# Kernel tuning notes

Measured on AMD Instinct MI355X. Metric: run time of the kernel, lower is better.

The kernel has to match this reference:

```python
import jax, jax.numpy as jnp
import numpy as np

DT = 0.01  # time_delta from init
SIGMA, RHO, BETA = 10.0, 28.0, 8.0 / 3.0  # Lorenz parameters for self.function


def setup_inputs() -> dict:
    key = jax.random.key(0)
    # traj: [T, len_var, B] ensemble of trajectory states over time
    traj = jax.random.normal(key, (2048, 3, 8192), dtype=jnp.float32)
    return {"traj": traj}


def _jacobian(state):
    # state: [V, B] -> discrete tangent map I + DT * J_lorenz(state), shape [B, V, V]
    x, y, z = state[0], state[1], state[2]
    zero = jnp.zeros_like(x)
    one = jnp.ones_like(x)
    J = jnp.stack([
        jnp.stack([-SIGMA * one, SIGMA * one, zero], axis=-1),
        jnp.stack([RHO - z, -one, -x], axis=-1),
        jnp.stack([y, x, -BETA * one], axis=-1),
    ], axis=-2)  # [B, V, V]
    return jnp.eye(3, dtype=state.dtype) + DT * J


def _gram_schmidt_rows(M):
    # Row-wise Gram-Schmidt + normalization, exactly as the torch gram_schmidt
    # (in-place slicing makes it modified GS against already-orthogonalized rows)
    # followed by normalization(). M: [B, V, V]. Returns (Q [B,V,V], lognorms [V,B]).
    V = M.shape[-2]
    rows, lognorms = [], []
    for k in range(V):
        r = M[..., k, :]
        for q in rows:  # q already unit-norm -> projection coeff is just q.r
            r = r - jnp.sum(q * r, axis=-1, keepdims=True) * q
        n = jnp.sqrt(jnp.sum(r * r, axis=-1, keepdims=True))
        rows.append(r / n)
        lognorms.append(jnp.log(n[..., 0]))
    return jnp.stack(rows, axis=-2), jnp.stack(lognorms, axis=0)


def reference(traj):
    T, V, B = traj.shape
    Q0 = jnp.broadcast_to(jnp.eye(V, dtype=traj.dtype), (B, V, V))

    def step(Q, state):
        M = jnp.einsum('bij,bjk->bik', _jacobian(state), Q)  # eye = Jaco @ eye
        Qn, ln = _gram_schmidt_rows(M)
        return Qn, ln

    _, lns = jax.lax.scan(step, Q0, traj)  # lns: [T, V, B]
    # Running-average recurrence L_{k+1} = (L_k*k*dt + log n_k)/((k+1)*dt)
    # telescopes exactly to sum_k log(n_k) / (T * dt).
    return jnp.sum(lns, axis=0) / (T * DT)  # [V, B] Lyapunov spectrum per trajectory
```

## Files before the change

kernel.cpp:

```cpp
#include <hip/hip_runtime.h>

#define T_STEPS 2048
#define B_CH    8192
#define DT_F    0.01f
#define CHUNK   128
#define WARM    64
#define NCHUNK  (T_STEPS / CHUNK)
#define TILE    8

__device__ __forceinline__ float fast_rsqrt(float x) { return __builtin_amdgcn_rsqf(x); }
__device__ __forceinline__ float fast_log2(float x)  { return __builtin_amdgcn_logf(x); }

struct Q9 { float q00,q01,q02,q10,q11,q12,q20,q21,q22; };

__device__ __forceinline__ void gs_step(float x, float y, float z, Q9& Q,
                                        float& S0, float& S1, float& S2) {
  const float a00 = 0.9f;
  const float a01 = 0.1f;
  const float a11 = 0.99f;
  const float a22 = 1.0f - DT_F * (8.0f / 3.0f);
  float a10 = DT_F * (28.0f - z);
  float a12 = -DT_F * x;
  float a20 = DT_F * y;
  float a21 = DT_F * x;

  float m00 = a00*Q.q00 + a01*Q.q10;
  float m01 = a00*Q.q01 + a01*Q.q11;
  float m02 = a00*Q.q02 + a01*Q.q12;
  float m10 = a10*Q.q00 + a11*Q.q10 + a12*Q.q20;
  float m11 = a10*Q.q01 + a11*Q.q11 + a12*Q.q21;
  float m12 = a10*Q.q02 + a11*Q.q12 + a12*Q.q22;
  float m20 = a20*Q.q00 + a21*Q.q10 + a22*Q.q20;
  float m21 = a20*Q.q01 + a21*Q.q11 + a22*Q.q21;
  float m22 = a20*Q.q02 + a21*Q.q12 + a22*Q.q22;

  float n0  = m00*m00 + m01*m01 + m02*m02;
  float d1u = m00*m10 + m01*m11 + m02*m12;
  float d2u = m00*m20 + m01*m21 + m02*m22;

  float i0 = fast_rsqrt(n0);
  float inv0 = i0 * i0;
  S0 += fast_log2(n0);
  Q.q00 = m00*i0; Q.q01 = m01*i0; Q.q02 = m02*i0;

  float c1 = d1u * inv0;
  float r10 = m10 - c1*m00, r11 = m11 - c1*m01, r12 = m12 - c1*m02;
  float c2 = d2u * inv0;
  float r20 = m20 - c2*m00, r21 = m21 - c2*m01, r22 = m22 - c2*m02;

  float n1 = r10*r10 + r11*r11 + r12*r12;
  float i1 = fast_rsqrt(n1);
  float inv1 = i1 * i1;
  S1 += fast_log2(n1);
  Q.q10 = r10*i1; Q.q11 = r11*i1; Q.q12 = r12*i1;

  float d3u = r10*r20 + r11*r21 + r12*r22;
  float c3 = d3u * inv1;
  float s20 = r20 - c3*r10, s21 = r21 - c3*r11, s22 = r22 - c3*r12;
  float n2 = s20*s20 + s21*s21 + s22*s22;
  float i2 = fast_rsqrt(n2);
  S2 += fast_log2(n2);
  Q.q20 = s20*i2; Q.q21 = s21*i2; Q.q22 = s22*i2;
}

__global__ __launch_bounds__(64) void lyap_chunk_kernel(const float* __restrict__ traj,
                                                        float* __restrict__ ws) {
  const int b = blockIdx.x * 64 + threadIdx.x;
  const int chunk = blockIdx.y;
  const int warm = (chunk == 0) ? 0 : WARM;
  const int warmTiles = warm / TILE;
  const int ntiles = (CHUNK + warm) / TILE;
  const float* __restrict__ p =
      traj + (size_t)(chunk * CHUNK - warm) * (3 * B_CH) + b;

  float sA[TILE][3], sB[TILE][3];
#pragma unroll
  for (int i = 0; i < TILE; ++i) {
    sA[i][0] = p[(i*3 + 0) * B_CH];
    sA[i][1] = p[(i*3 + 1) * B_CH];
    sA[i][2] = p[(i*3 + 2) * B_CH];
  }

  Q9 Q = {1.f,0.f,0.f, 0.f,1.f,0.f, 0.f,0.f,1.f};
  float S0 = 0.f, S1 = 0.f, S2 = 0.f;
  float B0 = 0.f, B1 = 0.f, B2 = 0.f;

  for (int t = 0; t < ntiles; t += 2) {
    {
      const float* pB = p + (size_t)(t + 1) * TILE * 3 * B_CH;
#pragma unroll
      for (int i = 0; i < TILE; ++i) {
        sB[i][0] = pB[(i*3 + 0) * B_CH];
        sB[i][1] = pB[(i*3 + 1) * B_CH];
        sB[i][2] = pB[(i*3 + 2) * B_CH];
      }
    }
    if (t == warmTiles) { B0 = S0; B1 = S1; B2 = S2; }
#pragma unroll
    for (int i = 0; i < TILE; ++i)
      gs_step(sA[i][0], sA[i][1], sA[i][2], Q, S0, S1, S2);

    if (t + 2 < ntiles) {
      const float* pA = p + (size_t)(t + 2) * TILE * 3 * B_CH;
#pragma unroll
      for (int i = 0; i < TILE; ++i) {
        sA[i][0] = pA[(i*3 + 0) * B_CH];
        sA[i][1] = pA[(i*3 + 1) * B_CH];
        sA[i][2] = pA[(i*3 + 2) * B_CH];
      }
    }
#pragma unroll
    for (int i = 0; i < TILE; ++i)
      gs_step(sB[i][0], sB[i][1], sB[i][2], Q, S0, S1, S2);
  }

  ws[(chunk*3 + 0) * B_CH + b] = S0 - B0;
  ws[(chunk*3 + 1) * B_CH + b] = S1 - B1;
  ws[(chunk*3 + 2) * B_CH + b] = S2 - B2;
}

__global__ __launch_bounds__(256) void lyap_reduce_kernel(const float* __restrict__ ws,
                                                          float* __restrict__ out) {
  const int i = blockIdx.x * 256 + threadIdx.x;
  float s = 0.f;
#pragma unroll
  for (int c = 0; c < NCHUNK; ++c) s += ws[c * 3 * B_CH + i];
  const float scale = 0.5f * 0.69314718055994531f / (T_STEPS * DT_F);
  out[i] = s * scale;
}

extern "C" void kernel_launch(void* const* d_in, const int* in_sizes, int n_in,
                              void* d_out, int out_size, void* d_ws, size_t ws_size,
                              hipStream_t stream) {
  (void)in_sizes; (void)n_in; (void)out_size; (void)ws_size;
  const float* traj = (const float*)d_in[0];
  float* out = (float*)d_out;
  float* ws  = (float*)d_ws;

  lyap_chunk_kernel<<<dim3(B_CH / 64, NCHUNK), dim3(64), 0, stream>>>(traj, ws);
  lyap_reduce_kernel<<<dim3(3 * B_CH / 256), dim3(256), 0, stream>>>(ws, out);
}
```

Baseline: 307.5 us.

## Batch log2 via running norm products and rebalance chunking to 32 chunks

```diff
diff --git a/kernel.cpp b/kernel.cpp
--- a/kernel.cpp
+++ b/kernel.cpp
@@ -3,18 +3,19 @@
 #define T_STEPS 2048
 #define B_CH    8192
 #define DT_F    0.01f
-#define CHUNK   128
+#define NCHUNK  32
+#define CHUNK   (T_STEPS / NCHUNK)
 #define WARM    64
-#define NCHUNK  (T_STEPS / CHUNK)
 #define TILE    8
 
+__device__ __forceinline__ float fast_rcp(float x)   { return __builtin_amdgcn_rcpf(x); }
 __device__ __forceinline__ float fast_rsqrt(float x) { return __builtin_amdgcn_rsqf(x); }
 __device__ __forceinline__ float fast_log2(float x)  { return __builtin_amdgcn_logf(x); }
 
 struct Q9 { float q00,q01,q02,q10,q11,q12,q20,q21,q22; };
 
 __device__ __forceinline__ void gs_step(float x, float y, float z, Q9& Q,
-                                        float& S0, float& S1, float& S2) {
+                                        float& P0, float& P1, float& P2) {
   const float a00 = 0.9f;
   const float a01 = 0.1f;
   const float a11 = 0.99f;
@@ -34,42 +35,42 @@
   float m21 = a20*Q.q01 + a21*Q.q11 + a22*Q.q21;
   float m22 = a20*Q.q02 + a21*Q.q12 + a22*Q.q22;
 
-  float n0  = m00*m00 + m01*m01 + m02*m02;
-  float d1u = m00*m10 + m01*m11 + m02*m12;
-  float d2u = m00*m20 + m01*m21 + m02*m22;
+  float n0 = m00*m00 + m01*m01 + m02*m02;
+  float d1 = m00*m10 + m01*m11 + m02*m12;
+  float d2 = m00*m20 + m01*m21 + m02*m22;
 
   float i0 = fast_rsqrt(n0);
   float inv0 = i0 * i0;
-  S0 += fast_log2(n0);
+  P0 *= n0;
   Q.q00 = m00*i0; Q.q01 = m01*i0; Q.q02 = m02*i0;
 
-  float c1 = d1u * inv0;
+  float c1 = d1 * inv0;
   float r10 = m10 - c1*m00, r11 = m11 - c1*m01, r12 = m12 - c1*m02;
-  float c2 = d2u * inv0;
+  float c2 = d2 * inv0;
   float r20 = m20 - c2*m00, r21 = m21 - c2*m01, r22 = m22 - c2*m02;
 
   float n1 = r10*r10 + r11*r11 + r12*r12;
+  float d3 = r10*r20 + r11*r21 + r12*r22;
   float i1 = fast_rsqrt(n1);
   float inv1 = i1 * i1;
-  S1 += fast_log2(n1);
+  P1 *= n1;
   Q.q10 = r10*i1; Q.q11 = r11*i1; Q.q12 = r12*i1;
 
-  float d3u = r10*r20 + r11*r21 + r12*r22;
-  float c3 = d3u * inv1;
+  float c3 = d3 * inv1;
   float s20 = r20 - c3*r10, s21 = r21 - c3*r11, s22 = r22 - c3*r12;
   float n2 = s20*s20 + s21*s21 + s22*s22;
   float i2 = fast_rsqrt(n2);
-  S2 += fast_log2(n2);
+  P2 *= n2;
   Q.q20 = s20*i2; Q.q21 = s21*i2; Q.q22 = s22*i2;
 }
 
-__global__ __launch_bounds__(64) void lyap_chunk_kernel(const float* __restrict__ traj,
-                                                        float* __restrict__ ws) {
-  const int b = blockIdx.x * 64 + threadIdx.x;
+__global__ __launch_bounds__(256, 4) void lyap_chunk_kernel(const float* __restrict__ traj,
+                                                            float* __restrict__ ws) {
+  const int b = blockIdx.x * 256 + threadIdx.x;
   const int chunk = blockIdx.y;
   const int warm = (chunk == 0) ? 0 : WARM;
-  const int warmTiles = warm / TILE;
-  const int ntiles = (CHUNK + warm) / TILE;
+  const int warmPer = warm / (2 * TILE);
+  const int nper = (CHUNK + warm) / (2 * TILE);
   const float* __restrict__ p =
       traj + (size_t)(chunk * CHUNK - warm) * (3 * B_CH) + b;
 
@@ -84,34 +85,39 @@
   Q9 Q = {1.f,0.f,0.f, 0.f,1.f,0.f, 0.f,0.f,1.f};
   float S0 = 0.f, S1 = 0.f, S2 = 0.f;
   float B0 = 0.f, B1 = 0.f, B2 = 0.f;
+  float P0 = 1.f, P1 = 1.f, P2 = 1.f;
 
-  for (int t = 0; t < ntiles; t += 2) {
+  for (int per = 0; per < nper; ++per) {
+    if (per == warmPer) { B0 = S0; B1 = S1; B2 = S2; }
     {
-      const float* pB = p + (size_t)(t + 1) * TILE * 3 * B_CH;
+      const float* pt = p + (size_t)(2*per + 1) * (TILE*3*B_CH);
 #pragma unroll
       for (int i = 0; i < TILE; ++i) {
-        sB[i][0] = pB[(i*3 + 0) * B_CH];
-        sB[i][1] = pB[(i*3 + 1) * B_CH];
-        sB[i][2] = pB[(i*3 + 2) * B_CH];
-      }
-    }
-    if (t == warmTiles) { B0 = S0; B1 = S1; B2 = S2; }
-#pragma unroll
-    for (int i = 0; i < TILE; ++i)
-      gs_step(sA[i][0], sA[i][1], sA[i][2], Q, S0, S1, S2);
-
-    if (t + 2 < ntiles) {
-      const float* pA = p + (size_t)(t + 2) * TILE * 3 * B_CH;
-#pragma unroll
-      for (int i = 0; i < TILE; ++i) {
-        sA[i][0] = pA[(i*3 + 0) * B_CH];
-        sA[i][1] = pA[(i*3 + 1) * B_CH];
-        sA[i][2] = pA[(i*3 + 2) * B_CH];
+        sB[i][0] = pt[(i*3 + 0) * B_CH];
+        sB[i][1] = pt[(i*3 + 1) * B_CH];
+        sB[i][2] = pt[(i*3 + 2) * B_CH];
       }
     }
 #pragma unroll
     for (int i = 0; i < TILE; ++i)
-      gs_step(sB[i][0], sB[i][1], sB[i][2], Q, S0, S1, S2);
+      gs_step(sA[i][0], sA[i][1], sA[i][2], Q, P0, P1, P2);
+
+    if (per + 1 < nper) {
+      const float* pt = p + (size_t)(2*per + 2) * (TILE*3*B_CH);
+#pragma unroll
+      for (int i = 0; i < TILE; ++i) {
+        sA[i][0] = pt[(i*3 + 0) * B_CH];
+        sA[i][1] = pt[(i*3 + 1) * B_CH];
+        sA[i][2] = pt[(i*3 + 2) * B_CH];
+      }
+    }
+#pragma unroll
+    for (int i = 0; i < TILE; ++i)
+      gs_step(sB[i][0], sB[i][1], sB[i][2], Q, P0, P1, P2);
+
+    S0 += fast_log2(P0); P0 = 1.f;
+    S1 += fast_log2(P1); P1 = 1.f;
+    S2 += fast_log2(P2); P2 = 1.f;
   }
 
   ws[(chunk*3 + 0) * B_CH + b] = S0 - B0;
@@ -137,6 +143,6 @@
   float* out = (float*)d_out;
   float* ws  = (float*)d_ws;
 
-  lyap_chunk_kernel<<<dim3(B_CH / 64, NCHUNK), dim3(64), 0, stream>>>(traj, ws);
+  lyap_chunk_kernel<<<dim3(B_CH / 256, NCHUNK), dim3(256), 0, stream>>>(traj, ws);
   lyap_reduce_kernel<<<dim3(3 * B_CH / 256), dim3(256), 0, stream>>>(ws, out);
 }
```

Result: slower. 314.0 us (+2.1%).
